# Kernel tuning notes

Measured on AMD Instinct MI355X. Metric: run time of the kernel, lower is better.

The kernel has to match this reference:

```python
import jax, jax.numpy as jnp
import numpy as np

LX, LY, D, PHYS = 8, 4, 4, 2
NN_ETA = 1e-3


def setup_inputs() -> dict:
    key = jax.random.key(0)
    ks = jax.random.split(key, 6)
    cfg = jax.random.randint(ks[0], (128, LX * LY), 0, 2)
    # PEPS site tensors [Lx, Ly, l, r, d, u, phys]; scaled small so the
    # Lx-long transfer-matrix product stays numerically moderate.
    A = 0.2 * jax.random.normal(ks[1], (LX, LY, D, D, D, D, PHYS), dtype=jnp.float32)
    W1 = jax.random.normal(ks[2], (LX * LY, 64), dtype=jnp.float32) * 0.1
    b1 = jax.random.normal(ks[3], (64,), dtype=jnp.float32) * 0.1
    W2 = jax.random.normal(ks[4], (64, 2 * LX * D * D * D * D * D), dtype=jnp.float32) * 0.05
    b2 = jax.random.normal(ks[5], (2 * LX * D * D * D * D * D,), dtype=jnp.float32) * 0.05
    return {"cfg": cfg, "A": A, "W1": W1, "b1": b1, "W2": W2, "b2": b2}


def reference(cfg, A, W1, b1, W2, b2):
    # A with phys axis moved up front of bond axes for gather: [Lx,Ly,phys,l,r,d,u]
    Ap = jnp.moveaxis(A, -1, 2)
    nb = LX * D * D * D * D * D  # flattened size of one (bottom or top) 2-row half

    def amp(c_flat):
        c = c_flat.reshape(LX, LY)
        # select physical index per site -> [Lx, Ly, l, r, d, u]
        s = jnp.take_along_axis(Ap, c[:, :, None, None, None, None, None], axis=2)[:, :, 0]
        # boundary contraction from ymin: merge rows 0,1 (bottom d-bond projected to 0)
        row0 = s[:, 0, :, :, 0, :]          # [Lx, l, r, u]
        row1 = s[:, 1]                       # [Lx, l, r, d, u]
        bot = jnp.einsum('xlru,xLRuU->xlLrRU', row0, row1).reshape(LX, D * D, D * D, D)
        # boundary contraction from ymax: merge rows 3,2 (top u-bond projected to 0)
        row3 = s[:, 3, :, :, :, 0]           # [Lx, l, r, d]
        row2 = s[:, 2]                       # [Lx, l, r, d, u]
        top = jnp.einsum('xlrdu,xLRu->xlLrRd', row2, row3).reshape(LX, D * D, D * D, D)
        # pack 2-row params into a vector, add MLP correction, unpack
        vec = jnp.concatenate([bot.reshape(-1), top.reshape(-1)])
        h = jax.nn.relu(c_flat.astype(jnp.float32) @ W1 + b1)
        vec = vec + NN_ETA * (h @ W2 + b2)
        bot2 = vec[:nb].reshape(LX, D * D, D * D, D)
        top2 = vec[nb:].reshape(LX, D * D, D * D, D)
        # column transfer matrices and open-boundary chain contraction
        M = jnp.einsum('xiju,xIJu->xiIjJ', bot2, top2).reshape(LX, D ** 4, D ** 4)
        v0 = jnp.zeros(D ** 4, dtype=vec.dtype).at[0].set(1.0)
        def step(v, m):
            return v @ m, None
        v, _ = jax.lax.scan(step, v0, M)
        return v[0]

    return jax.vmap(amp)(cfg)
```

## Files before the change

### kernel.cpp

```cpp
#include <hip/hip_runtime.h>

#define ETA 0.001f
#define NVEC 16384
#define NB   8192

__global__ __launch_bounds__(256) void nn_delta_kernel(
    const int* __restrict__ cfg, const float* __restrict__ W1,
    const float* __restrict__ b1, const float* __restrict__ W2,
    const float* __restrict__ b2, float* __restrict__ delta)
{
    __shared__ float Hs[16][64];
    const int t  = threadIdx.x;
    const int b0 = blockIdx.y * 16;
    const int n  = blockIdx.x * 256 + t;

    for (int e = t; e < 16 * 64; e += 256) {
        const int bb = e >> 6, k = e & 63;
        float acc = b1[k];
        const int* c = cfg + (b0 + bb) * 32;
        #pragma unroll
        for (int m = 0; m < 32; ++m)
            acc = fmaf((float)c[m], W1[m * 64 + k], acc);
        Hs[bb][k] = fmaxf(acc, 0.0f);
    }
    __syncthreads();

    float acc[16];
    #pragma unroll
    for (int bb = 0; bb < 16; ++bb) acc[bb] = 0.0f;

    #pragma unroll 4
    for (int k = 0; k < 64; ++k) {
        const float w = W2[k * NVEC + n];
        #pragma unroll
        for (int bb = 0; bb < 16; ++bb)
            acc[bb] = fmaf(Hs[bb][k], w, acc[bb]);
    }
    const float bias = b2[n];
    #pragma unroll
    for (int bb = 0; bb < 16; ++bb)
        delta[(b0 + bb) * NVEC + n] = ETA * (acc[bb] + bias);
}

__global__ __launch_bounds__(256) void contract_kernel(
    const int* __restrict__ cfg, const float* __restrict__ A,
    const float* __restrict__ delta, float* __restrict__ out)
{
    __shared__ float  s[8192];
    __shared__ float  vec[NVEC];
    __shared__ float4 T[256];
    __shared__ float  vbuf[2][256];
    __shared__ int    cfgs[32];

    const int t = threadIdx.x;
    const int b = blockIdx.x;

    if (t < 32) cfgs[t] = cfg[b * 32 + t];
    __syncthreads();

    for (int idx = t; idx < 8192; idx += 256)
        s[idx] = A[idx * 2 + cfgs[idx >> 8]];
    __syncthreads();

    const float4* dlt = (const float4*)(delta + b * NVEC);
    for (int q = 0; q < 16; ++q) {
        const int m    = q * 256 + t;
        const int half = m >> 11;
        const int x    = (m >> 8) & 7;
        const int i    = (m >> 4) & 15;
        const int j    = m & 15;
        const int l = i >> 2, L = i & 3, r = j >> 2, R = j & 3;
        const float* sA = s + (x * 4 + half * 2) * 256;
        const float* sB = sA + 256;

        float4 acc = make_float4(0.f, 0.f, 0.f, 0.f);
        if (half == 0) {
            #pragma unroll
            for (int u = 0; u < 4; ++u) {
                const float  a  = sA[l * 64 + r * 16 + u];
                const float4 bv = *(const float4*)(sB + L * 64 + R * 16 + u * 4);
                acc.x = fmaf(a, bv.x, acc.x);
                acc.y = fmaf(a, bv.y, acc.y);
                acc.z = fmaf(a, bv.z, acc.z);
                acc.w = fmaf(a, bv.w, acc.w);
            }
        } else {
            #pragma unroll
            for (int u = 0; u < 4; ++u) {
                const float bvs = sB[L * 64 + R * 16 + u * 4];
                const int base = l * 64 + r * 16;
                acc.x = fmaf(sA[base +  0 + u], bvs, acc.x);
                acc.y = fmaf(sA[base +  4 + u], bvs, acc.y);
                acc.z = fmaf(sA[base +  8 + u], bvs, acc.z);
                acc.w = fmaf(sA[base + 12 + u], bvs, acc.w);
            }
        }
        const float4 d4 = dlt[m];
        acc.x += d4.x; acc.y += d4.y; acc.z += d4.z; acc.w += d4.w;
        ((float4*)vec)[m] = acc;
    }
    __syncthreads();

    float* vcur = vbuf[0];
    float* vnxt = vbuf[1];
    vcur[t] = (t == 0) ? 1.0f : 0.0f;
    __syncthreads();

    const float4* bot4 = (const float4*)vec;
    const float4* top4 = (const float4*)(vec + NB);

    for (int x = 0; x < 8; ++x) {
        {
            const int I = t >> 4, j = t & 15;
            float4 acc = make_float4(0.f, 0.f, 0.f, 0.f);
            #pragma unroll
            for (int i = 0; i < 16; ++i) {
                const float  vi = vcur[i * 16 + I];
                const float4 bv = bot4[x * 256 + i * 16 + j];
                acc.x = fmaf(vi, bv.x, acc.x);
                acc.y = fmaf(vi, bv.y, acc.y);
                acc.z = fmaf(vi, bv.z, acc.z);
                acc.w = fmaf(vi, bv.w, acc.w);
            }
            T[t] = acc;
        }
        __syncthreads();
        {
            const int j = t >> 4, J = t & 15;
            float acc = 0.f;
            #pragma unroll
            for (int I = 0; I < 16; ++I) {
                const float4 tv = T[I * 16 + j];
                const float4 pv = top4[x * 256 + I * 16 + J];
                acc = fmaf(tv.x, pv.x, acc);
                acc = fmaf(tv.y, pv.y, acc);
                acc = fmaf(tv.z, pv.z, acc);
                acc = fmaf(tv.w, pv.w, acc);
            }
            vnxt[j * 16 + J] = acc;
        }
        __syncthreads();
        float* tmp = vcur; vcur = vnxt; vnxt = tmp;
    }

    if (t == 0) out[b] = vcur[0];
}

extern "C" void kernel_launch(void* const* d_in, const int* in_sizes, int n_in,
                              void* d_out, int out_size, void* d_ws, size_t ws_size,
                              hipStream_t stream) {
    const int*   cfg = (const int*)  d_in[0];
    const float* A   = (const float*)d_in[1];
    const float* W1  = (const float*)d_in[2];
    const float* b1  = (const float*)d_in[3];
    const float* W2  = (const float*)d_in[4];
    const float* b2  = (const float*)d_in[5];
    float* out   = (float*)d_out;
    float* delta = (float*)d_ws;

    const int ncfg = in_sizes[0] / 32;

    dim3 gA(NVEC / 256, ncfg / 16);
    nn_delta_kernel<<<gA, 256, 0, stream>>>(cfg, W1, b1, W2, b2, delta);
    contract_kernel<<<ncfg, 256, 0, stream>>>(cfg, A, delta, out);
}
```

Baseline: 89.68 us.

## Vectorize NN delta GEMM, prefetch delta into registers, transpose chain vector

The MLP-correction kernel now has each thread compute four output columns with float4 loads of W2, b2 and delta, over 8 configs per block instead of 16. The grid changes to match. In the contraction kernel, the per-config delta slice is prefetched into registers before the A gather so global latency overlaps. The cfg staging sync is removed and the half-split loops use wider LDS reads. The chain vector is stored transposed in a single buffer, so each thread reads its 16 inputs as float4 loads, at the cost of more registers and a possibly lower-occupancy NN kernel.

Result: slower. 96.10 us (+7.2%).

```diff
diff --git a/kernel.cpp b/kernel.cpp
--- a/kernel.cpp
+++ b/kernel.cpp
@@ -9,12 +9,12 @@
     const float* __restrict__ b1, const float* __restrict__ W2,
     const float* __restrict__ b2, float* __restrict__ delta)
 {
-    __shared__ float Hs[16][64];
+    __shared__ float Hs[8][64];
     const int t  = threadIdx.x;
-    const int b0 = blockIdx.y * 16;
-    const int n  = blockIdx.x * 256 + t;
+    const int b0 = blockIdx.y * 8;
+    const int n4 = blockIdx.x * 256 + t;
 
-    for (int e = t; e < 16 * 64; e += 256) {
+    for (int e = t; e < 8 * 64; e += 256) {
         const int bb = e >> 6, k = e & 63;
         float acc = b1[k];
         const int* c = cfg + (b0 + bb) * 32;
@@ -25,21 +25,34 @@
     }
     __syncthreads();
 
-    float acc[16];
+    float4 acc[8];
     #pragma unroll
-    for (int bb = 0; bb < 16; ++bb) acc[bb] = 0.0f;
+    for (int bb = 0; bb < 8; ++bb) acc[bb] = make_float4(0.f, 0.f, 0.f, 0.f);
 
+    const float4* W24 = (const float4*)W2;
     #pragma unroll 4
     for (int k = 0; k < 64; ++k) {
-        const float w = W2[k * NVEC + n];
+        const float4 w = W24[k * 4096 + n4];
         #pragma unroll
-        for (int bb = 0; bb < 16; ++bb)
-            acc[bb] = fmaf(Hs[bb][k], w, acc[bb]);
+        for (int bb = 0; bb < 8; ++bb) {
+            const float h = Hs[bb][k];
+            acc[bb].x = fmaf(h, w.x, acc[bb].x);
+            acc[bb].y = fmaf(h, w.y, acc[bb].y);
+            acc[bb].z = fmaf(h, w.z, acc[bb].z);
+            acc[bb].w = fmaf(h, w.w, acc[bb].w);
+        }
     }
-    const float bias = b2[n];
+    const float4 bias = ((const float4*)b2)[n4];
+    float4* d4 = (float4*)delta;
     #pragma unroll
-    for (int bb = 0; bb < 16; ++bb)
-        delta[(b0 + bb) * NVEC + n] = ETA * (acc[bb] + bias);
+    for (int bb = 0; bb < 8; ++bb) {
+        float4 r;
+        r.x = ETA * (acc[bb].x + bias.x);
+        r.y = ETA * (acc[bb].y + bias.y);
+        r.z = ETA * (acc[bb].z + bias.z);
+        r.w = ETA * (acc[bb].w + bias.w);
+        d4[(b0 + bb) * 4096 + n4] = r;
+    }
 }
 
 __global__ __launch_bounds__(256) void contract_kernel(
@@ -49,35 +62,37 @@
     __shared__ float  s[8192];
     __shared__ float  vec[NVEC];
     __shared__ float4 T[256];
-    __shared__ float  vbuf[2][256];
-    __shared__ int    cfgs[32];
+    __shared__ float  VT[256];
 
     const int t = threadIdx.x;
     const int b = blockIdx.x;
 
-    if (t < 32) cfgs[t] = cfg[b * 32 + t];
+    float4 dreg[16];
+    const float4* dlt = (const float4*)(delta + b * NVEC);
+    #pragma unroll
+    for (int q = 0; q < 16; ++q) dreg[q] = dlt[q * 256 + t];
+
+    const int* cb = cfg + b * 32;
+    for (int idx = t; idx < 8192; idx += 256)
+        s[idx] = A[idx * 2 + cb[idx >> 8]];
     __syncthreads();
 
-    for (int idx = t; idx < 8192; idx += 256)
-        s[idx] = A[idx * 2 + cfgs[idx >> 8]];
-    __syncthreads();
-
-    const float4* dlt = (const float4*)(delta + b * NVEC);
+    #pragma unroll
     for (int q = 0; q < 16; ++q) {
-        const int m    = q * 256 + t;
-        const int half = m >> 11;
-        const int x    = (m >> 8) & 7;
-        const int i    = (m >> 4) & 15;
-        const int j    = m & 15;
+        const int m = q * 256 + t;
+        const int x = (m >> 8) & 7;
+        const int i = (m >> 4) & 15;
+        const int j = m & 15;
         const int l = i >> 2, L = i & 3, r = j >> 2, R = j & 3;
-        const float* sA = s + (x * 4 + half * 2) * 256;
-        const float* sB = sA + 256;
 
         float4 acc = make_float4(0.f, 0.f, 0.f, 0.f);
-        if (half == 0) {
+        if (q < 8) {
+            const float* sA = s + (x * 4 + 0) * 256;
+            const float* sB = sA + 256;
+            const float4 a4 = *(const float4*)(sA + l * 64 + r * 16);
             #pragma unroll
             for (int u = 0; u < 4; ++u) {
-                const float  a  = sA[l * 64 + r * 16 + u];
+                const float  a  = (u == 0) ? a4.x : (u == 1) ? a4.y : (u == 2) ? a4.z : a4.w;
                 const float4 bv = *(const float4*)(sB + L * 64 + R * 16 + u * 4);
                 acc.x = fmaf(a, bv.x, acc.x);
                 acc.y = fmaf(a, bv.y, acc.y);
@@ -85,25 +100,29 @@
                 acc.w = fmaf(a, bv.w, acc.w);
             }
         } else {
-            #pragma unroll
-            for (int u = 0; u < 4; ++u) {
-                const float bvs = sB[L * 64 + R * 16 + u * 4];
-                const int base = l * 64 + r * 16;
-                acc.x = fmaf(sA[base +  0 + u], bvs, acc.x);
-                acc.y = fmaf(sA[base +  4 + u], bvs, acc.y);
-                acc.z = fmaf(sA[base +  8 + u], bvs, acc.z);
-                acc.w = fmaf(sA[base + 12 + u], bvs, acc.w);
-            }
+            const float* sA = s + (x * 4 + 2) * 256;
+            const float* sB = sA + 256;
+            const int baseB = L * 64 + R * 16;
+            const float4 bvs = make_float4(sB[baseB], sB[baseB + 4], sB[baseB + 8], sB[baseB + 12]);
+            const int baseA = l * 64 + r * 16;
+            const float4 r0 = *(const float4*)(sA + baseA);
+            const float4 r1 = *(const float4*)(sA + baseA + 4);
+            const float4 r2 = *(const float4*)(sA + baseA + 8);
+            const float4 r3 = *(const float4*)(sA + baseA + 12);
+            acc.x = fmaf(r0.x, bvs.x, fmaf(r0.y, bvs.y, fmaf(r0.z, bvs.z, r0.w * bvs.w)));
+            acc.y = fmaf(r1.x, bvs.x, fmaf(r1.y, bvs.y, fmaf(r1.z, bvs.z, r1.w * bvs.w)));
+            acc.z = fmaf(r2.x, bvs.x, fmaf(r2.y, bvs.y, fmaf(r2.z, bvs.z, r2.w * bvs.w)));
+            acc.w = fmaf(r3.x, bvs.x, fmaf(r3.y, bvs.y, fmaf(r3.z, bvs.z, r3.w * bvs.w)));
         }
-        const float4 d4 = dlt[m];
+        const float4 d4 = dreg[q];
         acc.x += d4.x; acc.y += d4.y; acc.z += d4.z; acc.w += d4.w;
         ((float4*)vec)[m] = acc;
     }
+
+
+    VT[t] = 0.0f;
     __syncthreads();
-
-    float* vcur = vbuf[0];
-    float* vnxt = vbuf[1];
-    vcur[t] = (t == 0) ? 1.0f : 0.0f;
+    if (t == 0) VT[0] = 1.0f;
     __syncthreads();
 
     const float4* bot4 = (const float4*)vec;
@@ -112,10 +131,15 @@
     for (int x = 0; x < 8; ++x) {
         {
             const int I = t >> 4, j = t & 15;
+            float vv[16];
+            *(float4*)&vv[0]  = *(const float4*)(VT + I * 16 + 0);
+            *(float4*)&vv[4]  = *(const float4*)(VT + I * 16 + 4);
+            *(float4*)&vv[8]  = *(const float4*)(VT + I * 16 + 8);
+            *(float4*)&vv[12] = *(const float4*)(VT + I * 16 + 12);
             float4 acc = make_float4(0.f, 0.f, 0.f, 0.f);
             #pragma unroll
             for (int i = 0; i < 16; ++i) {
-                const float  vi = vcur[i * 16 + I];
+                const float  vi = vv[i];
                 const float4 bv = bot4[x * 256 + i * 16 + j];
                 acc.x = fmaf(vi, bv.x, acc.x);
                 acc.y = fmaf(vi, bv.y, acc.y);
@@ -137,13 +161,12 @@
                 acc = fmaf(tv.z, pv.z, acc);
                 acc = fmaf(tv.w, pv.w, acc);
             }
-            vnxt[j * 16 + J] = acc;
+            VT[J * 16 + j] = acc;
         }
         __syncthreads();
-        float* tmp = vcur; vcur = vnxt; vnxt = tmp;
     }
 
-    if (t == 0) out[b] = vcur[0];
+    if (t == 0) out[b] = VT[0];
 }
 
 extern "C" void kernel_launch(void* const* d_in, const int* in_sizes, int n_in,
@@ -160,7 +183,7 @@
 
     const int ncfg = in_sizes[0] / 32;
 
-    dim3 gA(NVEC / 256, ncfg / 16);
+    dim3 gA(16, ncfg / 8);
     nn_delta_kernel<<<gA, 256, 0, stream>>>(cfg, W1, b1, W2, b2, delta);
     contract_kernel<<<ncfg, 256, 0, stream>>>(cfg, A, delta, out);
 }
```
